# Kernel tuning notes

Hardware: AMD Instinct MI355X
Metric: run time of the kernel (lower is better)

## Reference

```python
import jax, jax.numpy as jnp
import numpy as np

B, T, I, H = 64, 2048, 128, 256


def setup_inputs() -> dict:
    key = jax.random.key(0)
    k1, k2, k3 = jax.random.split(key, 3)
    inputs = jax.random.normal(k1, (B, T, I), dtype=jnp.float32)
    # 4 gates (input, forget, context, output), each an affine op on [x_t, h]
    W_x = jax.random.normal(k2, (4, I, H), dtype=jnp.float32) * (1.0 / np.sqrt(I))
    W_h = jax.random.normal(k3, (4, H, H), dtype=jnp.float32) * (1.0 / np.sqrt(H))
    b = jnp.zeros((4, H), dtype=jnp.float32)
    return {"inputs": inputs, "W_x": W_x, "W_h": W_h, "b": b}


def reference(inputs, W_x, W_h, b):
    # inputs: [B, T, I]; W_x: [4, I, H]; W_h: [4, H, H]; b: [4, H]
    Bb = inputs.shape[0]
    Hh = W_h.shape[-1]
    h0 = jnp.zeros((Bb, Hh), dtype=inputs.dtype)
    c0 = jnp.zeros((Bb, Hh), dtype=inputs.dtype)

    def step(carry, x_t):
        h, c = carry
        # all 4 gate pre-activations at once: [4, B, H]
        g = (jnp.einsum('bi,gih->gbh', x_t, W_x)
             + jnp.einsum('bh,ghk->gbk', h, W_h)
             + b[:, None, :])
        i_gate = jax.nn.sigmoid(g[0])
        f_gate = jax.nn.sigmoid(g[1])
        g_gate = jnp.tanh(g[2])
        o_gate = jax.nn.sigmoid(g[3])
        c_new = f_gate * c + i_gate * g_gate
        h_new = o_gate * jnp.tanh(c_new)
        return (h_new, c_new), h_new

    xs = jnp.swapaxes(inputs, 0, 1)  # [T, B, I]
    (_, _), hs = jax.lax.scan(step, (h0, c0), xs)  # hs: [T, B, H]
    return jnp.swapaxes(hs, 0, 1)  # [B, T, H]
```

## Files before the change

### kernel.cpp

```cpp
#include <hip/hip_runtime.h>
#include <hip/hip_bf16.h>


#define B_ 64
#define T_ 2048
#define I_ 128
#define H_ 256
#define NC 1024

typedef __attribute__((ext_vector_type(8))) short bf16x8;
typedef __attribute__((ext_vector_type(4))) float f32x4;
typedef __attribute__((ext_vector_type(4))) _Float16 f16x4;

static __device__ __forceinline__ unsigned short f2bf(float f) {
    unsigned u = __builtin_bit_cast(unsigned, f);
    u = (u + 0x7FFFu + ((u >> 16) & 1u)) >> 16;
    return (unsigned short)u;
}

static __device__ __forceinline__ int dot4(unsigned a, unsigned b, int c) {
#if __has_builtin(__builtin_amdgcn_sdot4)
    return __builtin_amdgcn_sdot4((int)a, (int)b, c, false);
#else
    int r = c;
    r += (int)(signed char)(a) * (int)(signed char)(b);
    r += (int)(signed char)(a >> 8) * (int)(signed char)(b >> 8);
    r += (int)(signed char)(a >> 16) * (int)(signed char)(b >> 16);
    r += (int)(signed char)(a >> 24) * (int)(signed char)(b >> 24);
    return r;
#endif
}

__global__ void pack_wh(const float* __restrict__ Wh, unsigned* __restrict__ wq,
                        float* __restrict__ sws) {
    int colp = blockIdx.x;
    int g = colp & 3, j = colp >> 2;
    int lane = threadIdx.x;
    float v[4];
    float m = 0.f;
#pragma unroll
    for (int u = 0; u < 4; ++u) {
        int k = lane * 4 + u;
        v[u] = Wh[(g * H_ + k) * H_ + j];
        m = fmaxf(m, fabsf(v[u]));
    }
#pragma unroll
    for (int off = 32; off; off >>= 1) m = fmaxf(m, __shfl_xor(m, off));
    float mm = (m > 0.f) ? m : 1.f;
    float inv = 127.f / mm;
    unsigned pack = 0;
#pragma unroll
    for (int u = 0; u < 4; ++u) {
        int q = (int)rintf(v[u] * inv);
        q = max(-127, min(127, q));
        pack |= ((unsigned)(q & 255)) << (8 * u);
    }
    wq[colp * 64 + lane] = pack;
    if (lane == 0) sws[colp] = mm / (127.f * 127.f);
}

__global__ void pack_wx(const float* __restrict__ Wx,
                        unsigned short* __restrict__ bxp) {
    int f = blockIdx.x * blockDim.x + threadIdx.x;
    int jj = f & 7;
    int colp = (f >> 3) & 1023;
    int c16 = f >> 13;
    int k = (c16 >> 2) * 32 + (c16 & 3) * 8 + jj;
    int g = colp & 3, h = colp >> 2;
    bxp[f] = f2bf(Wx[(g * I_ + k) * H_ + h]);
}

__global__ __launch_bounds__(256) void gemm_gx(
    const float* __restrict__ A, const unsigned short* __restrict__ Bp,
    unsigned short* __restrict__ Cg) {
    __shared__ uint4 sm[4096];
    int tid = threadIdx.x;
    int mt = blockIdx.x, nt = blockIdx.y;

    const float* Ab = A + (size_t)mt * 128 * I_;
    unsigned* dstA = (unsigned*)sm;
#pragma unroll
    for (int it = 0; it < 16; ++it) {
        int flat = it * 1024 + tid * 4;
        float4 a4 = *(const float4*)(Ab + flat);
        int m = flat >> 7, k0 = flat & 127;
        int c16 = k0 >> 3, j0 = k0 & 7;
        unsigned lo = (unsigned)f2bf(a4.x) | ((unsigned)f2bf(a4.y) << 16);
        unsigned hi = (unsigned)f2bf(a4.z) | ((unsigned)f2bf(a4.w) << 16);
        int didx = ((c16 * 128 + m) * 16 + j0 * 2) >> 2;
        dstA[didx] = lo;
        dstA[didx + 1] = hi;
    }
    const uint4* Bq = (const uint4*)Bp;
#pragma unroll
    for (int it = 0; it < 8; ++it) {
        int chunk = it * 2 + (tid >> 7);
        int inner = tid & 127;
        sm[2048 + chunk * 128 + inner] = Bq[chunk * 1024 + nt * 128 + inner];
    }
    __syncthreads();

    int wid = tid >> 6, lane = tid & 63;
    int r = lane & 15, q = lane >> 4;
    int mw = (wid & 1) * 64, nw = (wid >> 1) * 64;
    f32x4 acc[4][4] = {};
#pragma unroll
    for (int ki = 0; ki < 4; ++ki) {
        bf16x8 af[4], bfr[4];
#pragma unroll
        for (int x = 0; x < 4; ++x) {
            af[x] = __builtin_bit_cast(bf16x8,
                                       sm[(ki * 4 + q) * 128 + mw + x * 16 + r]);
            bfr[x] = __builtin_bit_cast(
                bf16x8, sm[2048 + (ki * 4 + q) * 128 + nw + x * 16 + r]);
        }
#pragma unroll
        for (int x = 0; x < 4; ++x)
#pragma unroll
            for (int y = 0; y < 4; ++y)
                acc[x][y] = __builtin_amdgcn_mfma_f32_16x16x32_bf16(
                    af[x], bfr[y], acc[x][y], 0, 0, 0);
    }
    __syncthreads();

    _Float16* ct = (_Float16*)sm;
#pragma unroll
    for (int x = 0; x < 4; ++x)
#pragma unroll
        for (int y = 0; y < 4; ++y)
#pragma unroll
            for (int g2 = 0; g2 < 4; ++g2) {
                int row = mw + x * 16 + q * 4 + g2;
                int colc = nw + y * 16 + r;
                ct[row * 128 + colc] = (_Float16)acc[x][y][g2];
            }
    __syncthreads();
    int m = tid >> 1, half = tid & 1;
    const uint4* src = (const uint4*)sm;
    uint4* dstg =
        (uint4*)(Cg + ((size_t)(mt * 128 + m) * NC + nt * 128 + half * 64));
#pragma unroll
    for (int i = 0; i < 8; ++i) dstg[i] = src[m * 16 + half * 8 + i];
}

__global__ __launch_bounds__(256, 1) void lstm_rec(
    const unsigned short* __restrict__ gx, const uint4* __restrict__ wq4,
    const float* __restrict__ sws, const float* __restrict__ bias,
    float* __restrict__ out) {
    int b = blockIdx.x, j = threadIdx.x;
    int lane = j & 63;

    unsigned w0[64], w1[64], w2[64], w3[64];
#pragma unroll
    for (int ii = 0; ii < 16; ++ii) {
        uint4 v0 = wq4[(j * 4 + 0) * 16 + ii];
        uint4 v1 = wq4[(j * 4 + 1) * 16 + ii];
        uint4 v2 = wq4[(j * 4 + 2) * 16 + ii];
        uint4 v3 = wq4[(j * 4 + 3) * 16 + ii];
        w0[4 * ii] = v0.x; w0[4 * ii + 1] = v0.y; w0[4 * ii + 2] = v0.z; w0[4 * ii + 3] = v0.w;
        w1[4 * ii] = v1.x; w1[4 * ii + 1] = v1.y; w1[4 * ii + 2] = v1.z; w1[4 * ii + 3] = v1.w;
        w2[4 * ii] = v2.x; w2[4 * ii + 1] = v2.y; w2[4 * ii + 2] = v2.z; w2[4 * ii + 3] = v2.w;
        w3[4 * ii] = v3.x; w3[4 * ii + 1] = v3.y; w3[4 * ii + 2] = v3.z; w3[4 * ii + 3] = v3.w;
    }
    float s0 = sws[j * 4 + 0], s1 = sws[j * 4 + 1];
    float s2 = sws[j * 4 + 2], s3 = sws[j * 4 + 3];
    float bb0 = bias[0 * H_ + j], bb1 = bias[1 * H_ + j];
    float bb2 = bias[2 * H_ + j], bb3 = bias[3 * H_ + j];

    __shared__ unsigned hbuf[2][64];
    if (j < 64) hbuf[0][j] = 0u;
    __syncthreads();

    float c = 0.f;
    const _Float16* gxh = (const _Float16*)gx;
    size_t rowbase = (size_t)b * T_;
    f16x4 gv = *(const f16x4*)(gxh + rowbase * NC + j * 4);

    for (int t = 0; t < T_; ++t) {
        size_t row = rowbase + t;
        f16x4 nv = *(const f16x4*)(gxh + (row + 1) * NC + j * 4);

        unsigned hd = hbuf[t & 1][lane];
        int a0 = 0, a1 = 0, a2 = 0, a3 = 0;
#pragma unroll
        for (int i = 0; i < 64; ++i) {
            unsigned hs = (unsigned)__builtin_amdgcn_readlane((int)hd, i);
            a0 = dot4(hs, w0[i], a0);
            a1 = dot4(hs, w1[i], a1);
            a2 = dot4(hs, w2[i], a2);
            a3 = dot4(hs, w3[i], a3);
        }
        float g0 = (float)a0 * s0 + (float)gv.x + bb0;
        float g1 = (float)a1 * s1 + (float)gv.y + bb1;
        float g2 = (float)a2 * s2 + (float)gv.z + bb2;
        float g3 = (float)a3 * s3 + (float)gv.w + bb3;

        float ig = 1.f / (1.f + __expf(-g0));
        float fg = 1.f / (1.f + __expf(-g1));
        float gg = 2.f / (1.f + __expf(-2.f * g2)) - 1.f;
        float og = 1.f / (1.f + __expf(-g3));
        c = fg * c + ig * gg;
        float th = 2.f / (1.f + __expf(-2.f * c)) - 1.f;
        float h = og * th;
        out[row * H_ + j] = h;
        int qv = (int)rintf(h * 127.f);
        ((signed char*)hbuf[(t + 1) & 1])[j] = (signed char)qv;
        __syncthreads();
        gv = nv;
    }
}

extern "C" void kernel_launch(void* const* d_in, const int* in_sizes, int n_in,
                              void* d_out, int out_size, void* d_ws,
                              size_t ws_size, hipStream_t stream) {
    const float* inputs = (const float*)d_in[0];
    const float* Wx = (const float*)d_in[1];
    const float* Wh = (const float*)d_in[2];
    const float* bias = (const float*)d_in[3];
    float* out = (float*)d_out;

    char* ws = (char*)d_ws;
    unsigned short* gxbuf = (unsigned short*)ws;
    size_t off = (size_t)B_ * T_ * NC * 2;
    unsigned* wq = (unsigned*)(ws + off);
    off += (size_t)NC * 64 * 4;
    float* sws = (float*)(ws + off);
    off += (size_t)NC * 4;
    unsigned short* bxp = (unsigned short*)(ws + off);
    off += (size_t)I_ * NC * 2;

    pack_wh<<<NC, 64, 0, stream>>>(Wh, wq, sws);
    pack_wx<<<(I_ * NC) / 256, 256, 0, stream>>>(Wx, bxp);
    gemm_gx<<<dim3((B_ * T_) / 128, NC / 128), 256, 0, stream>>>(inputs, bxp,
                                                                 gxbuf);
    lstm_rec<<<B_, 256, 0, stream>>>(gxbuf, (const uint4*)wq, sws, bias, out);
}
```

Measured before the change: 2.603 ms.

## Split LSTM gate columns across two half-waves and fold bias into input GEMM

New measurement: 2.893 ms. +11.1%, slower.

```diff
diff --git a/kernel.cpp b/kernel.cpp
--- a/kernel.cpp
+++ b/kernel.cpp
@@ -10,7 +10,7 @@
 
 typedef __attribute__((ext_vector_type(8))) short bf16x8;
 typedef __attribute__((ext_vector_type(4))) float f32x4;
-typedef __attribute__((ext_vector_type(4))) _Float16 f16x4;
+typedef __attribute__((ext_vector_type(2))) _Float16 f16x2;
 
 static __device__ __forceinline__ unsigned short f2bf(float f) {
     unsigned u = __builtin_bit_cast(unsigned, f);
@@ -31,10 +31,16 @@
 #endif
 }
 
-__global__ void pack_wh(const float* __restrict__ Wh, unsigned* __restrict__ wq,
-                        float* __restrict__ sws) {
+static __device__ __forceinline__ int slotmap(int x) {
+    return ((x & 1) << 1) | (x >> 1);
+}
+
+__global__ void pack_wh(const float* __restrict__ Wh, const float* __restrict__ b,
+                        unsigned* __restrict__ wq, float* __restrict__ sws,
+                        float* __restrict__ biasP) {
     int colp = blockIdx.x;
-    int g = colp & 3, j = colp >> 2;
+    int slot = colp & 3, j = colp >> 2;
+    int g = slotmap(slot);
     int lane = threadIdx.x;
     float v[4];
     float m = 0.f;
@@ -56,7 +62,10 @@
         pack |= ((unsigned)(q & 255)) << (8 * u);
     }
     wq[colp * 64 + lane] = pack;
-    if (lane == 0) sws[colp] = mm / (127.f * 127.f);
+    if (lane == 0) {
+        sws[colp] = mm / (127.f * 127.f);
+        biasP[colp] = b[g * H_ + j];
+    }
 }
 
 __global__ void pack_wx(const float* __restrict__ Wx,
@@ -66,13 +75,14 @@
     int colp = (f >> 3) & 1023;
     int c16 = f >> 13;
     int k = (c16 >> 2) * 32 + (c16 & 3) * 8 + jj;
-    int g = colp & 3, h = colp >> 2;
+    int slot = colp & 3, h = colp >> 2;
+    int g = slotmap(slot);
     bxp[f] = f2bf(Wx[(g * I_ + k) * H_ + h]);
 }
 
 __global__ __launch_bounds__(256) void gemm_gx(
     const float* __restrict__ A, const unsigned short* __restrict__ Bp,
-    unsigned short* __restrict__ Cg) {
+    const float* __restrict__ biasP, unsigned short* __restrict__ Cg) {
     __shared__ uint4 sm[4096];
     int tid = threadIdx.x;
     int mt = blockIdx.x, nt = blockIdx.y;
@@ -121,6 +131,9 @@
                 acc[x][y] = __builtin_amdgcn_mfma_f32_16x16x32_bf16(
                     af[x], bfr[y], acc[x][y], 0, 0, 0);
     }
+    float bv[4];
+#pragma unroll
+    for (int y = 0; y < 4; ++y) bv[y] = biasP[nt * 128 + nw + y * 16 + r];
     __syncthreads();
 
     _Float16* ct = (_Float16*)sm;
@@ -132,7 +145,7 @@
             for (int g2 = 0; g2 < 4; ++g2) {
                 int row = mw + x * 16 + q * 4 + g2;
                 int colc = nw + y * 16 + r;
-                ct[row * 128 + colc] = (_Float16)acc[x][y][g2];
+                ct[row * 128 + colc] = (_Float16)(acc[x][y][g2] + bv[y]);
             }
     __syncthreads();
     int m = tid >> 1, half = tid & 1;
@@ -143,70 +156,73 @@
     for (int i = 0; i < 8; ++i) dstg[i] = src[m * 16 + half * 8 + i];
 }
 
-__global__ __launch_bounds__(256, 1) void lstm_rec(
+__global__ __launch_bounds__(512, 2) void lstm_rec(
     const unsigned short* __restrict__ gx, const uint4* __restrict__ wq4,
-    const float* __restrict__ sws, const float* __restrict__ bias,
-    float* __restrict__ out) {
-    int b = blockIdx.x, j = threadIdx.x;
-    int lane = j & 63;
-
-    unsigned w0[64], w1[64], w2[64], w3[64];
+    const float* __restrict__ sws, float* __restrict__ out) {
+    int b = blockIdx.x, tid = threadIdx.x;
+    int w = tid >> 6, lane = tid & 63;
+    int half = lane >> 5;
+    int j = w * 32 + (lane & 31);
+    int colA = j * 4 + half * 2;
+
+    unsigned wA[64], wB[64];
 #pragma unroll
     for (int ii = 0; ii < 16; ++ii) {
-        uint4 v0 = wq4[(j * 4 + 0) * 16 + ii];
-        uint4 v1 = wq4[(j * 4 + 1) * 16 + ii];
-        uint4 v2 = wq4[(j * 4 + 2) * 16 + ii];
-        uint4 v3 = wq4[(j * 4 + 3) * 16 + ii];
-        w0[4 * ii] = v0.x; w0[4 * ii + 1] = v0.y; w0[4 * ii + 2] = v0.z; w0[4 * ii + 3] = v0.w;
-        w1[4 * ii] = v1.x; w1[4 * ii + 1] = v1.y; w1[4 * ii + 2] = v1.z; w1[4 * ii + 3] = v1.w;
-        w2[4 * ii] = v2.x; w2[4 * ii + 1] = v2.y; w2[4 * ii + 2] = v2.z; w2[4 * ii + 3] = v2.w;
-        w3[4 * ii] = v3.x; w3[4 * ii + 1] = v3.y; w3[4 * ii + 2] = v3.z; w3[4 * ii + 3] = v3.w;
-    }
-    float s0 = sws[j * 4 + 0], s1 = sws[j * 4 + 1];
-    float s2 = sws[j * 4 + 2], s3 = sws[j * 4 + 3];
-    float bb0 = bias[0 * H_ + j], bb1 = bias[1 * H_ + j];
-    float bb2 = bias[2 * H_ + j], bb3 = bias[3 * H_ + j];
+        uint4 vA = wq4[(size_t)colA * 16 + ii];
+        uint4 vB = wq4[(size_t)(colA + 1) * 16 + ii];
+        wA[4 * ii] = vA.x; wA[4 * ii + 1] = vA.y; wA[4 * ii + 2] = vA.z; wA[4 * ii + 3] = vA.w;
+        wB[4 * ii] = vB.x; wB[4 * ii + 1] = vB.y; wB[4 * ii + 2] = vB.z; wB[4 * ii + 3] = vB.w;
+    }
+    float sA = sws[colA], sB = sws[colA + 1];
 
     __shared__ unsigned hbuf[2][64];
-    if (j < 64) hbuf[0][j] = 0u;
+    if (tid < 64) hbuf[0][tid] = 0u;
     __syncthreads();
 
     float c = 0.f;
-    const _Float16* gxh = (const _Float16*)gx;
-    size_t rowbase = (size_t)b * T_;
-    f16x4 gv = *(const f16x4*)(gxh + rowbase * NC + j * 4);
-
-    for (int t = 0; t < T_; ++t) {
-        size_t row = rowbase + t;
-        f16x4 nv = *(const f16x4*)(gxh + (row + 1) * NC + j * 4);
-
-        unsigned hd = hbuf[t & 1][lane];
-        int a0 = 0, a1 = 0, a2 = 0, a3 = 0;
-#pragma unroll
-        for (int i = 0; i < 64; ++i) {
-            unsigned hs = (unsigned)__builtin_amdgcn_readlane((int)hd, i);
-            a0 = dot4(hs, w0[i], a0);
-            a1 = dot4(hs, w1[i], a1);
-            a2 = dot4(hs, w2[i], a2);
-            a3 = dot4(hs, w3[i], a3);
+    const _Float16* gp = (const _Float16*)gx + (size_t)b * T_ * NC + colA;
+    float* op = out + (size_t)b * T_ * H_ + j;
+
+    for (int tb = 0; tb < T_; tb += 8) {
+        f16x2 gbuf[8];
+#pragma unroll
+        for (int s = 0; s < 8; ++s)
+            gbuf[s] = *(const f16x2*)(gp + (size_t)(tb + s) * NC);
+        float hsave[8];
+#pragma unroll
+        for (int s = 0; s < 8; ++s) {
+            int par = s & 1;
+            unsigned hd = hbuf[par][lane];
+            int aA = 0, aB = 0;
+#pragma unroll
+            for (int i = 0; i < 64; ++i) {
+                unsigned hs = (unsigned)__builtin_amdgcn_readlane((int)hd, i);
+                aA = dot4(hs, wA[i], aA);
+                aB = dot4(hs, wB[i], aB);
+            }
+            float gA = (float)aA * sA + (float)gbuf[s].x;
+            float gB = (float)aB * sB + (float)gbuf[s].y;
+            float sigA = 1.f / (1.f + __expf(-gA));
+            float p = 0.f;
+            if (half == 0) {
+                float tg = 2.f / (1.f + __expf(-2.f * gB)) - 1.f;
+                p = sigA * tg;
+            }
+            float pr = __shfl_xor(p, 32);
+            if (half) {
+                float og = 1.f / (1.f + __expf(-gB));
+                c = sigA * c + pr;
+                float th = 2.f / (1.f + __expf(-2.f * c) ) - 1.f;
+                float h = og * th;
+                hsave[s] = h;
+                ((signed char*)hbuf[par ^ 1])[j] = (signed char)(int)rintf(h * 127.f);
+            }
+            __syncthreads();
         }
-        float g0 = (float)a0 * s0 + (float)gv.x + bb0;
-        float g1 = (float)a1 * s1 + (float)gv.y + bb1;
-        float g2 = (float)a2 * s2 + (float)gv.z + bb2;
-        float g3 = (float)a3 * s3 + (float)gv.w + bb3;
-
-        float ig = 1.f / (1.f + __expf(-g0));
-        float fg = 1.f / (1.f + __expf(-g1));
-        float gg = 2.f / (1.f + __expf(-2.f * g2)) - 1.f;
-        float og = 1.f / (1.f + __expf(-g3));
-        c = fg * c + ig * gg;
-        float th = 2.f / (1.f + __expf(-2.f * c)) - 1.f;
-        float h = og * th;
-        out[row * H_ + j] = h;
-        int qv = (int)rintf(h * 127.f);
-        ((signed char*)hbuf[(t + 1) & 1])[j] = (signed char)qv;
-        __syncthreads();
-        gv = nv;
+        if (half) {
+#pragma unroll
+            for (int s = 0; s < 8; ++s) op[(size_t)(tb + s) * H_] = hsave[s];
+        }
     }
 }
 
@@ -226,12 +242,14 @@
     off += (size_t)NC * 64 * 4;
     float* sws = (float*)(ws + off);
     off += (size_t)NC * 4;
+    float* biasP = (float*)(ws + off);
+    off += (size_t)NC * 4;
     unsigned short* bxp = (unsigned short*)(ws + off);
     off += (size_t)I_ * NC * 2;
 
-    pack_wh<<<NC, 64, 0, stream>>>(Wh, wq, sws);
+    pack_wh<<<NC, 64, 0, stream>>>(Wh, bias, wq, sws, biasP);
     pack_wx<<<(I_ * NC) / 256, 256, 0, stream>>>(Wx, bxp);
     gemm_gx<<<dim3((B_ * T_) / 128, NC / 128), 256, 0, stream>>>(inputs, bxp,
-                                                                 gxbuf);
-    lstm_rec<<<B_, 256, 0, stream>>>(gxbuf, (const uint4*)wq, sws, bias, out);
-}
+                                                                 biasP, gxbuf);
+    lstm_rec<<<B_, 512, 0, stream>>>(gxbuf, (const uint4*)wq, sws, out);
+}
```
